# Performance work log

Measured on AMD Instinct MI355X. Metric: run time of the kernel, lower is better.

## Reference

```python
import jax, jax.numpy as jnp
import numpy as np

N_VOX = (128, 128, 8)            # (X, Y, Z) voxels
D_BINS = 66                      # int((50 - 0) / 0.75)
DEPTH_RANGE = (0.0, 50.0)
IMG_H, IMG_W = 512.0, 1408.0     # img_pad_shape / img_shape (features are stride-16: 32x88)
PC_RANGE = (-51.2, -51.2, -5.0, 51.2, 51.2, 3.0)


def _make_points():
    # voxel-center anchors, laid out so reshape(n_voxels[::-1]+[-1]) = [Z,Y,X,C] (x fastest)
    nx, ny, nz = N_VOX
    x0, y0, z0, x1, y1, z1 = PC_RANGE
    xc = x0 + (np.arange(nx) + 0.5) * (x1 - x0) / nx
    yc = y0 + (np.arange(ny) + 0.5) * (y1 - y0) / ny
    zc = z0 + (np.arange(nz) + 0.5) * (z1 - z0) / nz
    zz, yy, xx = np.meshgrid(zc, yc, xc, indexing='ij')
    return np.stack([xx, yy, zz], -1).reshape(-1, 3).astype(np.float32)


def _make_proj(B, N):
    # realistic ori_lidar2img: pinhole K @ [R|t], six surround cameras 60 deg apart
    K = np.array([[560., 0., 704., 0.], [0., 560., 256., 0.],
                  [0., 0., 1., 0.], [0., 0., 0., 1.]], np.float64)
    mats = []
    for n in range(N):
        th = 2.0 * np.pi * n / N
        fwd = np.array([np.cos(th), np.sin(th), 0.0])
        right = np.array([np.sin(th), -np.cos(th), 0.0])
        down = np.array([0.0, 0.0, -1.0])
        Rt = np.eye(4)
        Rt[:3, :3] = np.stack([right, down, fwd])
        Rt[:3, 3] = [0.0, 0.2, 0.0]
        mats.append(K @ Rt)
    P = np.stack(mats).astype(np.float32)
    return np.broadcast_to(P, (B, N, 4, 4)).copy()


def setup_inputs() -> dict:
    key = jax.random.key(0)
    B, N, C, H, W = 1, 6, 64, 32, 88
    k1, k2, k3 = jax.random.split(key, 3)
    return {
        'x_fov': jax.random.normal(k1, (B, N, C, H, W), jnp.float32),
        'w_dn': jax.random.normal(k2, (C + D_BINS, C), jnp.float32) * 0.05,
        'b_dn': jax.random.normal(k3, (C + D_BINS,), jnp.float32) * 0.05,
        'points': jnp.asarray(_make_points()),
        'proj_mats': jnp.asarray(_make_proj(B, N)),
    }


def _trilinear(vol, gx, gy, gz):
    # vol: [C, D, H, W]; gx/gy/gz: [P] continuous indices along W/H/D
    # grid_sample(align_corners=False, padding_mode='zeros') semantics
    C, D, H, W = vol.shape
    x0f, y0f, z0f = jnp.floor(gx), jnp.floor(gy), jnp.floor(gz)
    tx, ty, tz = gx - x0f, gy - y0f, gz - z0f
    x0, y0, z0 = x0f.astype(jnp.int32), y0f.astype(jnp.int32), z0f.astype(jnp.int32)
    out = jnp.zeros((C, gx.shape[0]), vol.dtype)
    for dz, wz in ((0, 1.0 - tz), (1, tz)):
        for dy, wy in ((0, 1.0 - ty), (1, ty)):
            for dx, wx in ((0, 1.0 - tx), (1, tx)):
                xi, yi, zi = x0 + dx, y0 + dy, z0 + dz
                inb = ((xi >= 0) & (xi < W) & (yi >= 0) & (yi < H)
                       & (zi >= 0) & (zi < D))
                w = (wx * wy * wz) * inb.astype(vol.dtype)  # [P]
                corner = vol[:, jnp.clip(zi, 0, D - 1),
                             jnp.clip(yi, 0, H - 1),
                             jnp.clip(xi, 0, W - 1)]        # [C, P]
                out = out + corner * w
    return out.T  # [P, C]


def reference(x_fov, w_dn, b_dn, points, proj_mats):
    B, N, C, H, W = x_fov.shape
    nx, ny, nz = N_VOX
    dr0, dr1 = DEPTH_RANGE
    # 1x1 conv depth_net
    y = jnp.einsum('bnchw,oc->bnohw', x_fov, w_dn) + b_dn[None, None, :, None, None]
    depth = jax.nn.softmax(y[:, :, :D_BINS], axis=2)       # [B,N,D,H,W]
    feat = y[:, :, D_BINS:]                                # [B,N,C,H,W]
    # LSS outer product -> [B,N,C,D,H,W]
    vol = depth[:, :, None] * feat[:, :, :, None]
    # project voxel centers into each camera
    hom = jnp.concatenate([points, jnp.ones_like(points[:, :1])], -1)  # [P,4]
    pts = jnp.einsum('bnij,pj->bnpi', proj_mats, hom)      # [B,N,P,4]
    z = pts[..., 2]
    zs = jnp.where(jnp.abs(z) > 1e-3, z, 1e-3)
    u = pts[..., 0] / zs
    v = pts[..., 1] / zs
    valid = ((u >= 0) & (u < IMG_W) & (v >= 0) & (v < IMG_H)
             & (z > dr0) & (z < dr1))                      # [B,N,P]
    # normalized->index coords (align_corners=False): idx = norm01*size - 0.5
    gx = u / IMG_W * W - 0.5
    gy = v / IMG_H * H - 0.5
    gz = (z - dr0) / (dr1 - dr0) * D_BINS - 0.5
    P = points.shape[0]
    samp = jax.vmap(_trilinear)(vol.reshape(B * N, C, D_BINS, H, W),
                                gx.reshape(B * N, P),
                                gy.reshape(B * N, P),
                                gz.reshape(B * N, P))      # [B*N,P,C]
    samp = samp.reshape(B, N, P, C) * valid[..., None].astype(samp.dtype)
    counts = valid.astype(samp.dtype).sum(1)               # [B,P]
    ssum = samp.sum(1)                                     # [B,P,C]
    out = jnp.where(counts[..., None] > 0,
                    ssum / jnp.clip(counts, 1e-3, None)[..., None],
                    jnp.zeros_like(ssum))
    # [B,P,C] -> [B,Z,Y,X,C] -> [B,C,X,Y,Z]
    return out.reshape(B, nz, ny, nx, C).transpose(0, 4, 3, 2, 1)
```

## Files before the change

kernel.cpp:

```cpp
#include <hip/hip_runtime.h>
#include <math.h>

#define NCAM 6
#define CCH  64
#define DB   66
#define FH   32
#define FW   88
#define NX   128
#define NY   128
#define NZ   8
#define NPTS (NX*NY*NZ)
#define NPIX (NCAM*FH*FW)
#define PPC  (FH*FW)

#define TPX   32
#define DN_T  256
#define WS2   132
#define YSS   35
#define OFF_XS 0
#define OFF_WT 2048
#define OFF_YS 2048
#define OFF_BS 10496
#define LDS_F  10626

__global__ __launch_bounds__(DN_T) void depthnet_kernel(
    const float* __restrict__ x_fov, const float* __restrict__ w_dn,
    const float* __restrict__ b_dn, float* __restrict__ feat_t,
    float* __restrict__ depth_t)
{
    __shared__ float lds[LDS_F];
    float* xs = lds + OFF_XS;
    float* wT = lds + OFF_WT;
    float* ys = lds + OFF_YS;
    float* bs = lds + OFF_BS;

    const int t   = threadIdx.x;
    const int T   = blockIdx.x * TPX;
    const int cam = T / PPC;
    const int ph0 = T - cam * PPC;

    if (t < DB + CCH) bs[t] = b_dn[t];
    for (int i = t; i < (DB + CCH) * CCH; i += DN_T) {
        const int o = i >> 6, c = i & 63;
        wT[c * WS2 + o] = w_dn[i];
    }
    {
        const float* xb = x_fov + (size_t)cam * CCH * PPC + ph0;
        const int c = t >> 2;
        const int q = t & 3;
        #pragma unroll
        for (int h = 0; h < 2; ++h) {
            const float4 v = *(const float4*)(xb + c * PPC + h * 16 + q * 4);
            *(float4*)(xs + c * TPX + h * 16 + q * 4) = v;
        }
    }
    __syncthreads();

    const int pq = t & 3;
    const int oq = t >> 2;
    float acc[2][8];
    float acc2[2][8];
    #pragma unroll
    for (int a = 0; a < 2; ++a)
        #pragma unroll
        for (int p = 0; p < 8; ++p) { acc[a][p] = 0.f; acc2[a][p] = 0.f; }

    {
        const float* xr  = xs + pq * 8;
        const float* wr  = wT + oq * 2;
        const float* wr2 = wT + 128;
        #pragma unroll 4
        for (int c = 0; c < 64; ++c) {
            const float4 xa = *(const float4*)(xr + c * TPX);
            const float4 xb2 = *(const float4*)(xr + c * TPX + 4);
            const float2 wv = *(const float2*)(wr + c * WS2);
            const float xv[8] = {xa.x, xa.y, xa.z, xa.w, xb2.x, xb2.y, xb2.z, xb2.w};
            #pragma unroll
            for (int p = 0; p < 8; ++p) {
                acc[0][p] += wv.x * xv[p];
                acc[1][p] += wv.y * xv[p];
            }
            if (oq == 0) {
                const float2 w2 = *(const float2*)(wr2 + c * WS2);
                #pragma unroll
                for (int p = 0; p < 8; ++p) {
                    acc2[0][p] += w2.x * xv[p];
                    acc2[1][p] += w2.y * xv[p];
                }
            }
        }
    }
    __syncthreads();

    #pragma unroll
    for (int a = 0; a < 2; ++a) {
        const int o = 2 * oq + a;
        const float b = bs[o];
        #pragma unroll
        for (int p = 0; p < 8; ++p) ys[o * YSS + pq * 8 + p] = acc[a][p] + b;
    }
    if (oq == 0) {
        #pragma unroll
        for (int a = 0; a < 2; ++a) {
            const int o = 128 + a;
            const float b = bs[o];
            #pragma unroll
            for (int p = 0; p < 8; ++p) ys[o * YSS + pq * 8 + p] = acc2[a][p] + b;
        }
    }
    __syncthreads();

    {
        const int spx = t >> 3;
        const int r   = t & 7;
        float m = -1e30f;
        #pragma unroll
        for (int i = 0; i < 9; ++i) {
            const int o = r + 8 * i;
            if (o < DB) m = fmaxf(m, ys[o * YSS + spx]);
        }
        m = fmaxf(m, __shfl_xor(m, 1));
        m = fmaxf(m, __shfl_xor(m, 2));
        m = fmaxf(m, __shfl_xor(m, 4));
        float e[9];
        float ssum = 0.f;
        #pragma unroll
        for (int i = 0; i < 9; ++i) {
            const int o = r + 8 * i;
            const float v = (o < DB) ? expf(ys[o * YSS + spx] - m) : 0.f;
            e[i] = v;
            ssum += v;
        }
        ssum += __shfl_xor(ssum, 1);
        ssum += __shfl_xor(ssum, 2);
        ssum += __shfl_xor(ssum, 4);
        const float inv = 1.f / ssum;
        #pragma unroll
        for (int i = 0; i < 9; ++i) {
            const int o = r + 8 * i;
            if (o < DB) depth_t[(size_t)(T + spx) * DB + o] = e[i] * inv;
        }
    }

    for (int i = t; i < TPX * CCH; i += DN_T) {
        const int px = i >> 6, o = i & 63;
        feat_t[(size_t)T * CCH + i] = ys[(DB + o) * YSS + px];
    }
}

__global__ __launch_bounds__(256) void splat_kernel(
    const float* __restrict__ feat_t, const float* __restrict__ depth_t,
    const float* __restrict__ proj, float* __restrict__ out)
{
    __shared__ float trans[64 * 33];
    const int t    = threadIdx.x;
    const int w    = t >> 6;
    const int lane = t & 63;
    const int g    = lane >> 3;
    const int s    = lane & 7;
    const int gb   = lane & 56;
    const int ix   = blockIdx.x >> 5;
    const int iy0  = 4 * (blockIdx.x & 31);
    const int iy   = iy0 + w;

    const double DXY = 102.4 / 128.0;
    const float px = (float)(-51.2 + (ix + 0.5) * DXY);
    const float py = (float)(-51.2 + (iy + 0.5) * DXY);
    const float pz = (float)(-5.0 + (g + 0.5) * 1.0);

    float gxs = 0.f, gys = 0.f, gzs = -1e3f;
    bool validm = false;
    if (s < NCAM) {
        const float* M = proj + s * 16;
        const float u4 = M[0] * px + M[1] * py + M[2]  * pz + M[3];
        const float v4 = M[4] * px + M[5] * py + M[6]  * pz + M[7];
        const float z  = M[8] * px + M[9] * py + M[10] * pz + M[11];
        const float zs = fabsf(z) > 0.001f ? z : 0.001f;
        const float u = u4 / zs;
        const float v = v4 / zs;
        validm = (u >= 0.f) && (u < 1408.f) && (v >= 0.f) && (v < 512.f) &&
                 (z > 0.f) && (z < 50.f);
        if (validm) {
            gxs = u / 1408.0f * (float)FW - 0.5f;
            gys = v / 512.0f  * (float)FH - 0.5f;
            gzs = z / 50.0f   * (float)DB - 0.5f;
        }
    }
    const unsigned long long bal = __ballot(validm);
    const float cnt = (float)__popcll((bal >> (g * 8)) & 0x3Full);

    float acc[8];
    #pragma unroll
    for (int a = 0; a < 8; ++a) acc[a] = 0.f;

    for (int cam = 0; cam < NCAM; ++cam) {
        const float gx = __shfl(gxs, gb | cam);
        const float gy = __shfl(gys, gb | cam);
        const float gz = __shfl(gzs, gb | cam);
        if (gz < -500.f) continue;

        const float xf = floorf(gx), yf = floorf(gy), zf = floorf(gz);
        const float tx = gx - xf, ty = gy - yf, tz = gz - zf;
        const int x0 = (int)xf, y0 = (int)yf, z0 = (int)zf;

        const float wz0 = (z0 >= 0 && z0 < DB) ? (1.f - tz) : 0.f;
        const float wz1 = (z0 + 1 < DB) ? tz : 0.f;
        const int zi0 = min(max(z0, 0), DB - 1);
        const int zi1 = min(max(z0 + 1, 0), DB - 1);

        float wcorn[4];
        int   pixc[4];
        #pragma unroll
        for (int dy = 0; dy < 2; ++dy) {
            const int yi = y0 + dy;
            const bool yin = (yi >= 0) & (yi < FH);
            const int yic = min(max(yi, 0), FH - 1);
            const float wy = (dy ? ty : 1.f - ty) * (yin ? 1.f : 0.f);
            #pragma unroll
            for (int dx = 0; dx < 2; ++dx) {
                const int xi = x0 + dx;
                const bool xin = (xi >= 0) & (xi < FW);
                const int xic = min(max(xi, 0), FW - 1);
                const float wx = (dx ? tx : 1.f - tx) * (xin ? 1.f : 0.f);
                wcorn[2 * dy + dx] = wx * wy;
                pixc[2 * dy + dx]  = (cam * FH + yic) * FW + xic;
            }
        }

        const int kc = s & 3;
        const float* dptr = depth_t + (size_t)pixc[kc] * DB;
        const float wl = wcorn[kc] * (wz0 * dptr[zi0] + wz1 * dptr[zi1]);
        const float w0 = __shfl(wl, gb | 0);
        const float w1 = __shfl(wl, gb | 1);
        const float w2 = __shfl(wl, gb | 2);
        const float w3 = __shfl(wl, gb | 3);
        const float wcs[4] = {w0, w1, w2, w3};

        #pragma unroll
        for (int k = 0; k < 4; ++k) {
            const float wc = wcs[k];
            const float* fb = feat_t + (size_t)pixc[k] * CCH + s * 4;
            const float4 fa = *(const float4*)(fb);
            const float4 fh = *(const float4*)(fb + 32);
            acc[0] += wc * fa.x; acc[1] += wc * fa.y;
            acc[2] += wc * fa.z; acc[3] += wc * fa.w;
            acc[4] += wc * fh.x; acc[5] += wc * fh.y;
            acc[6] += wc * fh.z; acc[7] += wc * fh.w;
        }
    }

    const float invc = cnt > 0.f ? 1.f / cnt : 0.f;
    #pragma unroll
    for (int j = 0; j < 4; ++j) {
        trans[(4 * s + j) * 33 + w * 8 + g]      = acc[j]     * invc;
        trans[(32 + 4 * s + j) * 33 + w * 8 + g] = acc[4 + j] * invc;
    }
    __syncthreads();
    {
        const int idx = t & 31;
        const int cb  = t >> 5;
        const size_t obase = (size_t)ix * (NY * NZ) + iy0 * 8 + idx;
        #pragma unroll
        for (int i = 0; i < 8; ++i) {
            const int c = cb + 8 * i;
            out[(size_t)c * NPTS + obase] = trans[c * 33 + idx];
        }
    }
}

extern "C" void kernel_launch(void* const* d_in, const int* in_sizes, int n_in,
                              void* d_out, int out_size, void* d_ws, size_t ws_size,
                              hipStream_t stream) {
    const float* x_fov = (const float*)d_in[0];
    const float* w_dn  = (const float*)d_in[1];
    const float* b_dn  = (const float*)d_in[2];
    const float* proj  = (const float*)d_in[4];
    float* out = (float*)d_out;

    float* feat_t  = (float*)d_ws;
    float* depth_t = feat_t + (size_t)NPIX * CCH;

    depthnet_kernel<<<NPIX / TPX, DN_T, 0, stream>>>(x_fov, w_dn, b_dn, feat_t, depth_t);

    splat_kernel<<<(NX * NY) / 4, 256, 0, stream>>>(feat_t, depth_t, proj, out);
}
```

Measured before the change: 101.4 us.

## Rewrite depthnet as per-pixel register GEMV with depth-major layout

Measured after the change: 148.1 us. +46.0%, slower.

```diff
diff --git a/kernel.cpp b/kernel.cpp
--- a/kernel.cpp
+++ b/kernel.cpp
@@ -13,143 +13,64 @@
 #define NPIX (NCAM*FH*FW)
 #define PPC  (FH*FW)
 
-#define TPX   32
-#define DN_T  256
-#define WS2   132
-#define YSS   35
-#define OFF_XS 0
-#define OFF_WT 2048
-#define OFF_YS 2048
-#define OFF_BS 10496
-#define LDS_F  10626
-
-__global__ __launch_bounds__(DN_T) void depthnet_kernel(
+__global__ __launch_bounds__(256, 1) void depthnet_kernel(
     const float* __restrict__ x_fov, const float* __restrict__ w_dn,
     const float* __restrict__ b_dn, float* __restrict__ feat_t,
-    float* __restrict__ depth_t)
+    float* __restrict__ depth_T)
 {
-    __shared__ float lds[LDS_F];
-    float* xs = lds + OFF_XS;
-    float* wT = lds + OFF_WT;
-    float* ys = lds + OFF_YS;
-    float* bs = lds + OFF_BS;
-
-    const int t   = threadIdx.x;
-    const int T   = blockIdx.x * TPX;
-    const int cam = T / PPC;
-    const int ph0 = T - cam * PPC;
-
-    if (t < DB + CCH) bs[t] = b_dn[t];
-    for (int i = t; i < (DB + CCH) * CCH; i += DN_T) {
-        const int o = i >> 6, c = i & 63;
-        wT[c * WS2 + o] = w_dn[i];
-    }
-    {
-        const float* xb = x_fov + (size_t)cam * CCH * PPC + ph0;
-        const int c = t >> 2;
-        const int q = t & 3;
-        #pragma unroll
-        for (int h = 0; h < 2; ++h) {
-            const float4 v = *(const float4*)(xb + c * PPC + h * 16 + q * 4);
-            *(float4*)(xs + c * TPX + h * 16 + q * 4) = v;
+    __shared__ float fl[128 * 65];
+    const int t    = threadIdx.x;
+    const int wid  = t >> 6;
+    const int lane = t & 63;
+    const int pxl  = (wid & 1) * 64 + lane;
+    const int pg   = blockIdx.x * 128 + pxl;
+    const int cam  = blockIdx.x / 22;
+    const int p    = pg - cam * PPC;
+
+    const float* xf = x_fov + (size_t)cam * CCH * PPC + p;
+    float x[64];
+    #pragma unroll
+    for (int c = 0; c < 64; ++c) x[c] = xf[(size_t)c * PPC];
+
+    if (wid < 2) {
+        float y[DB];
+        #pragma unroll
+        for (int o = 0; o < DB; ++o) {
+            float a = b_dn[o];
+            #pragma unroll
+            for (int c = 0; c < 64; ++c) a = fmaf(w_dn[o * 64 + c], x[c], a);
+            y[o] = a;
+        }
+        float m = y[0];
+        #pragma unroll
+        for (int o = 1; o < DB; ++o) m = fmaxf(m, y[o]);
+        float ssum = 0.f;
+        #pragma unroll
+        for (int o = 0; o < DB; ++o) { y[o] = expf(y[o] - m); ssum += y[o]; }
+        const float inv = 1.f / ssum;
+        #pragma unroll
+        for (int o = 0; o < DB; ++o)
+            depth_T[(size_t)o * NPIX + pg] = y[o] * inv;
+    } else {
+        #pragma unroll
+        for (int o = 0; o < CCH; ++o) {
+            float a = b_dn[DB + o];
+            #pragma unroll
+            for (int c = 0; c < 64; ++c) a = fmaf(w_dn[(DB + o) * 64 + c], x[c], a);
+            fl[pxl * 65 + o] = a;
         }
     }
     __syncthreads();
 
-    const int pq = t & 3;
-    const int oq = t >> 2;
-    float acc[2][8];
-    float acc2[2][8];
-    #pragma unroll
-    for (int a = 0; a < 2; ++a)
-        #pragma unroll
-        for (int p = 0; p < 8; ++p) { acc[a][p] = 0.f; acc2[a][p] = 0.f; }
-
-    {
-        const float* xr  = xs + pq * 8;
-        const float* wr  = wT + oq * 2;
-        const float* wr2 = wT + 128;
-        #pragma unroll 4
-        for (int c = 0; c < 64; ++c) {
-            const float4 xa = *(const float4*)(xr + c * TPX);
-            const float4 xb2 = *(const float4*)(xr + c * TPX + 4);
-            const float2 wv = *(const float2*)(wr + c * WS2);
-            const float xv[8] = {xa.x, xa.y, xa.z, xa.w, xb2.x, xb2.y, xb2.z, xb2.w};
-            #pragma unroll
-            for (int p = 0; p < 8; ++p) {
-                acc[0][p] += wv.x * xv[p];
-                acc[1][p] += wv.y * xv[p];
-            }
-            if (oq == 0) {
-                const float2 w2 = *(const float2*)(wr2 + c * WS2);
-                #pragma unroll
-                for (int p = 0; p < 8; ++p) {
-                    acc2[0][p] += w2.x * xv[p];
-                    acc2[1][p] += w2.y * xv[p];
-                }
-            }
-        }
-    }
-    __syncthreads();
-
-    #pragma unroll
-    for (int a = 0; a < 2; ++a) {
-        const int o = 2 * oq + a;
-        const float b = bs[o];
-        #pragma unroll
-        for (int p = 0; p < 8; ++p) ys[o * YSS + pq * 8 + p] = acc[a][p] + b;
-    }
-    if (oq == 0) {
-        #pragma unroll
-        for (int a = 0; a < 2; ++a) {
-            const int o = 128 + a;
-            const float b = bs[o];
-            #pragma unroll
-            for (int p = 0; p < 8; ++p) ys[o * YSS + pq * 8 + p] = acc2[a][p] + b;
-        }
-    }
-    __syncthreads();
-
-    {
-        const int spx = t >> 3;
-        const int r   = t & 7;
-        float m = -1e30f;
-        #pragma unroll
-        for (int i = 0; i < 9; ++i) {
-            const int o = r + 8 * i;
-            if (o < DB) m = fmaxf(m, ys[o * YSS + spx]);
-        }
-        m = fmaxf(m, __shfl_xor(m, 1));
-        m = fmaxf(m, __shfl_xor(m, 2));
-        m = fmaxf(m, __shfl_xor(m, 4));
-        float e[9];
-        float ssum = 0.f;
-        #pragma unroll
-        for (int i = 0; i < 9; ++i) {
-            const int o = r + 8 * i;
-            const float v = (o < DB) ? expf(ys[o * YSS + spx] - m) : 0.f;
-            e[i] = v;
-            ssum += v;
-        }
-        ssum += __shfl_xor(ssum, 1);
-        ssum += __shfl_xor(ssum, 2);
-        ssum += __shfl_xor(ssum, 4);
-        const float inv = 1.f / ssum;
-        #pragma unroll
-        for (int i = 0; i < 9; ++i) {
-            const int o = r + 8 * i;
-            if (o < DB) depth_t[(size_t)(T + spx) * DB + o] = e[i] * inv;
-        }
-    }
-
-    for (int i = t; i < TPX * CCH; i += DN_T) {
+    const size_t fbase = (size_t)blockIdx.x * 128 * CCH;
+    for (int i = t; i < 128 * CCH; i += 256) {
         const int px = i >> 6, o = i & 63;
-        feat_t[(size_t)T * CCH + i] = ys[(DB + o) * YSS + px];
+        feat_t[fbase + i] = fl[px * 65 + o];
     }
 }
 
 __global__ __launch_bounds__(256) void splat_kernel(
-    const float* __restrict__ feat_t, const float* __restrict__ depth_t,
+    const float* __restrict__ feat_t, const float* __restrict__ depth_T,
     const float* __restrict__ proj, float* __restrict__ out)
 {
     __shared__ float trans[64 * 33];
@@ -228,8 +149,9 @@
         }
 
         const int kc = s & 3;
-        const float* dptr = depth_t + (size_t)pixc[kc] * DB;
-        const float wl = wcorn[kc] * (wz0 * dptr[zi0] + wz1 * dptr[zi1]);
+        const float t0 = depth_T[(size_t)zi0 * NPIX + pixc[kc]];
+        const float t1 = depth_T[(size_t)zi1 * NPIX + pixc[kc]];
+        const float wl = wcorn[kc] * (wz0 * t0 + wz1 * t1);
         const float w0 = __shfl(wl, gb | 0);
         const float w1 = __shfl(wl, gb | 1);
         const float w2 = __shfl(wl, gb | 2);
@@ -278,9 +200,9 @@
     float* out = (float*)d_out;
 
     float* feat_t  = (float*)d_ws;
-    float* depth_t = feat_t + (size_t)NPIX * CCH;
-
-    depthnet_kernel<<<NPIX / TPX, DN_T, 0, stream>>>(x_fov, w_dn, b_dn, feat_t, depth_t);
-
-    splat_kernel<<<(NX * NY) / 4, 256, 0, stream>>>(feat_t, depth_t, proj, out);
+    float* depth_T = feat_t + (size_t)NPIX * CCH;
+
+    depthnet_kernel<<<132, 256, 0, stream>>>(x_fov, w_dn, b_dn, feat_t, depth_T);
+
+    splat_kernel<<<(NX * NY) / 4, 256, 0, stream>>>(feat_t, depth_T, proj, out);
 }
```
